# Performance work log

Measured on AMD Instinct MI355X. Metric: run time of the kernel, lower is better.

The kernel has to match this reference:

```python
import jax, jax.numpy as jnp
import numpy as np
from jax import lax

B, D, H, W = 16, 256, 64, 64
P = 8  # patchsize
EPS = 1e-5


def setup_inputs() -> dict:
    key = jax.random.key(0)
    ks = jax.random.split(key, 8)
    s = 0.02
    return {
        "x": jax.random.normal(ks[0], (B, D, H, W), jnp.float32),
        "wq": jax.random.normal(ks[1], (D, D), jnp.float32) * s,
        "bq": jnp.zeros((D,), jnp.float32),
        "wk": jax.random.normal(ks[2], (D, D), jnp.float32) * s,
        "bk": jnp.zeros((D,), jnp.float32),
        "wv": jax.random.normal(ks[3], (D, D), jnp.float32) * s,
        "bv": jnp.zeros((D,), jnp.float32),
        "w_out": jax.random.normal(ks[4], (D, D, 3, 3), jnp.float32) * s,
        "b_out": jnp.zeros((D,), jnp.float32),
        "gamma": jnp.ones((D,), jnp.float32),
        "beta": jnp.zeros((D,), jnp.float32),
        "bn_mean": jnp.zeros((D,), jnp.float32),
        "bn_var": jnp.ones((D,), jnp.float32),
    }


def _conv1x1(x, w, b):
    # x: [b,c,h,w], w: [o,c] (1x1 conv) -> [b,o,h,w]
    return jnp.einsum('bchw,oc->bohw', x, w) + b[None, :, None, None]


def _to_patches(t, p):
    # [b,d,h,w] -> [b, p*p, d*hh*ww]  (matches view+permute(0,2,4,1,3,5)+view)
    b, d, h, w = t.shape
    hh, ww = h // p, w // p
    t = t.reshape(b, d, p, hh, p, ww).transpose(0, 2, 4, 1, 3, 5)
    return t.reshape(b, p * p, d * hh * ww)


def reference(x, wq, bq, wk, bk, wv, bv, w_out, b_out, gamma, beta, bn_mean, bn_var):
    b, d, h, w = x.shape
    p = P
    hh, ww = h // p, w // p

    q = _to_patches(_conv1x1(x, wq, bq), p)  # [b, p^2, d*hh*ww]
    k = _to_patches(_conv1x1(x, wk, bk), p)
    v = _to_patches(_conv1x1(x, wv, bv), p)

    scale = 1.0 / jnp.sqrt(jnp.asarray(q.shape[-1], q.dtype))
    scores = jnp.einsum('bqe,bke->bqk', q, k) * scale  # [b, p^2, p^2]
    attn = jax.nn.softmax(scores, axis=-1)
    out = jnp.einsum('bqk,bke->bqe', attn, v)  # [b, p^2, d*hh*ww]

    # [b,p,p,d,hh,ww] -> permute(0,3,1,4,2,5) -> [b,d,h,w]
    out = out.reshape(b, p, p, d, hh, ww).transpose(0, 3, 1, 4, 2, 5).reshape(b, d, h, w)

    # 3x3 conv, padding 1
    y = lax.conv_general_dilated(out, w_out, window_strides=(1, 1),
                                 padding=((1, 1), (1, 1)),
                                 dimension_numbers=('NCHW', 'OIHW', 'NCHW'))
    y = y + b_out[None, :, None, None]

    # BatchNorm2d (eval mode with running stats)
    inv = gamma / jnp.sqrt(bn_var + EPS)
    y = (y - bn_mean[None, :, None, None]) * inv[None, :, None, None] + beta[None, :, None, None]

    # LeakyReLU(0.2)
    return jnp.where(y >= 0, y, 0.2 * y)
```

## Files before the change

### kernel.cpp

```cpp
#include <hip/hip_runtime.h>
#include <hip/hip_bf16.h>

#define BB 16
#define SS 4096

typedef __attribute__((ext_vector_type(8))) short short8;
typedef __attribute__((ext_vector_type(4))) float float4v;

__global__ __launch_bounds__(256) void wprep_qkv(
    const float* __restrict__ wq, const float* __restrict__ wk,
    const float* __restrict__ wv, __hip_bfloat16* __restrict__ blob) {
  int chunk = blockIdx.x * 256 + threadIdx.x;
  int lane = chunk & 63;
  int ob = (chunk >> 6) & 15;
  int cb = (chunk >> 10) & 7;
  int which = chunk >> 13;
  const float* W = (which == 0) ? wq : (which == 1) ? wk : wv;
  int o = ob * 16 + (lane & 15);
  int c0 = cb * 32 + (lane >> 4) * 8;
  const float* p = W + o * 256 + c0;
  union { uint4 u; __hip_bfloat16 h[8]; } t;
#pragma unroll
  for (int j = 0; j < 8; ++j) t.h[j] = __float2bfloat16(p[j]);
  *reinterpret_cast<uint4*>(blob + (size_t)chunk * 8) = t.u;
}

__global__ __launch_bounds__(256) void qkv_mfma(
    const float* __restrict__ x, const __hip_bfloat16* __restrict__ blob,
    const float* __restrict__ bq, const float* __restrict__ bk,
    const float* __restrict__ bv,
    __hip_bfloat16* __restrict__ qb, __hip_bfloat16* __restrict__ kb,
    __hip_bfloat16* __restrict__ vb) {
  __shared__ short ls[2][64 * 40];
  const int which = blockIdx.z;
  const int b = blockIdx.y;
  const int s0 = blockIdx.x * 64;
  const float* bias = (which == 0) ? bq : (which == 1) ? bk : bv;
  __hip_bfloat16* outb = (which == 0) ? qb : kb;
  const int tid = threadIdx.x;
  const int wave = tid >> 6, lane = tid & 63;
  const int q = lane >> 4, m = lane & 15;
  const int sl = tid & 63;
  const int cg = tid >> 6;
  float4v acc[4][4] = {};

  const float* xbase = x + ((size_t)(b * 256 + cg * 8)) * SS + s0 + sl;
  float xr[8];
#pragma unroll
  for (int i = 0; i < 8; ++i) xr[i] = xbase[(size_t)i * SS];
  {
    union { uint4 u; __hip_bfloat16 h[8]; } t;
#pragma unroll
    for (int i = 0; i < 8; ++i) t.h[i] = __float2bfloat16(xr[i]);
    *reinterpret_cast<uint4*>(&ls[0][sl * 40 + cg * 8]) = t.u;
  }
  __syncthreads();

  for (int cb = 0; cb < 8; ++cb) {
    const short* cur = ls[cb & 1];
    short* nxt = ls[(cb + 1) & 1];
    if (cb < 7) {
#pragma unroll
      for (int i = 0; i < 8; ++i)
        xr[i] = xbase[(size_t)(cb + 1) * 32 * SS + (size_t)i * SS];
    }
    short8 af[4];
#pragma unroll
    for (int of = 0; of < 4; ++of)
      af[of] = *reinterpret_cast<const short8*>(
          blob +
          ((size_t)(((which * 8 + cb) * 16 + wave * 4 + of) * 64 + lane)) * 8);
    short8 xf[4];
#pragma unroll
    for (int sf = 0; sf < 4; ++sf)
      xf[sf] =
          *reinterpret_cast<const short8*>(&cur[(sf * 16 + m) * 40 + q * 8]);
#pragma unroll
    for (int of = 0; of < 4; ++of)
#pragma unroll
      for (int sf = 0; sf < 4; ++sf)
        acc[of][sf] = __builtin_amdgcn_mfma_f32_16x16x32_bf16(
            af[of], xf[sf], acc[of][sf], 0, 0, 0);
    if (cb < 7) {
      union { uint4 u; __hip_bfloat16 h[8]; } t;
#pragma unroll
      for (int i = 0; i < 8; ++i) t.h[i] = __float2bfloat16(xr[i]);
      *reinterpret_cast<uint4*>(&nxt[sl * 40 + cg * 8]) = t.u;
    }
    __syncthreads();
  }
  if (which == 2) {
    const int h = s0 >> 6;
#pragma unroll
    for (int of = 0; of < 4; ++of) {
      int o_base = wave * 64 + of * 16 + q * 4;
#pragma unroll
      for (int sf = 0; sf < 4; ++sf) {
        int w = sf * 16 + m;
        union { uint2 u; __hip_bfloat16 hh[4]; } t;
#pragma unroll
        for (int r = 0; r < 4; ++r)
          t.hh[r] = __float2bfloat16(acc[of][sf][r] + bias[o_base + r]);
        *reinterpret_cast<uint2*>(
            vb + ((size_t)((b * 64 + h) * 64 + w)) * 256 + o_base) = t.u;
      }
    }
  } else {
#pragma unroll
    for (int of = 0; of < 4; ++of) {
      int o_base = wave * 64 + of * 16 + q * 4;
#pragma unroll
      for (int r = 0; r < 4; ++r) {
        int o = o_base + r;
        float bi = bias[o];
        __hip_bfloat16* op = outb + ((size_t)(b * 256 + o)) * SS + s0 + m;
#pragma unroll
        for (int sf = 0; sf < 4; ++sf)
          op[sf * 16] = __float2bfloat16(acc[of][sf][r] + bi);
      }
    }
  }
}

__global__ __launch_bounds__(256) void scores_mfma(
    const __hip_bfloat16* __restrict__ qb, const __hip_bfloat16* __restrict__ kb,
    float* __restrict__ part) {
  const int b = blockIdx.y;
  const int d0 = blockIdx.x * 8;
  const int tid = threadIdx.x;
  const int wave = tid >> 6, lane = tid & 63;
  const int q = lane >> 4, m = lane & 15;
  const int t = wave * 16 + m;
  const int arow = (t >> 3) * 8;
  const int acol = (t & 7) * 8;
  float4v acc[4] = {};

  for (int dd = 0; dd < 8; ++dd) {
    const int d = d0 + dd;
    const __hip_bfloat16* qp = qb + ((size_t)(b * 256 + d)) * SS;
    const __hip_bfloat16* kp = kb + ((size_t)(b * 256 + d)) * SS;
#pragma unroll
    for (int khalf = 0; khalf < 2; ++khalf) {
      const int oh = khalf * 4 + q;
      short8 af = *reinterpret_cast<const short8*>(
          qp + (arow + oh) * 64 + acol);
      short8 bf[4];
#pragma unroll
      for (int nt = 0; nt < 4; ++nt) {
        int tp = nt * 16 + m;
        bf[nt] = *reinterpret_cast<const short8*>(
            kp + ((tp >> 3) * 8 + oh) * 64 + (tp & 7) * 8);
      }
#pragma unroll
      for (int nt = 0; nt < 4; ++nt)
        acc[nt] = __builtin_amdgcn_mfma_f32_16x16x32_bf16(af, bf[nt], acc[nt],
                                                          0, 0, 0);
    }
  }
  float* pp = part + ((size_t)(blockIdx.x * BB + b)) * 4096;
#pragma unroll
  for (int nt = 0; nt < 4; ++nt)
#pragma unroll
    for (int r = 0; r < 4; ++r)
      pp[(wave * 16 + q * 4 + r) * 64 + nt * 16 + m] = acc[nt][r];
}

__global__ __launch_bounds__(64) void softmax_kernel(
    const float* __restrict__ part, __hip_bfloat16* __restrict__ attnb) {
  const int t = blockIdx.x;
  const int b = blockIdx.y;
  const int lane = threadIdx.x;
  float v = 0.f;
#pragma unroll
  for (int sl = 0; sl < 32; ++sl)
    v += part[((size_t)(sl * BB + b)) * 4096 + t * 64 + lane];
  v *= 0.0078125f;
  float m = v;
#pragma unroll
  for (int off = 32; off >= 1; off >>= 1) m = fmaxf(m, __shfl_xor(m, off));
  float e = __expf(v - m);
  float s = e;
#pragma unroll
  for (int off = 32; off >= 1; off >>= 1) s += __shfl_xor(s, off);
  attnb[(b * 64 + t) * 64 + lane] = __float2bfloat16(e / s);
}

__global__ __launch_bounds__(256) void apply_mfma(
    const __hip_bfloat16* __restrict__ attnb, const __hip_bfloat16* __restrict__ vb,
    __hip_bfloat16* __restrict__ zb) {
  __shared__ short Vs[64][268];
  const int off = blockIdx.x;
  const int b = blockIdx.y;
  const int oh = off >> 3, ow = off & 7;
  const int tid = threadIdx.x;
#pragma unroll
  for (int i = 0; i < 8; ++i) {
    int chunk = i * 256 + tid;
    int tp = chunk >> 5;
    int cg = chunk & 31;
    int hh = (tp >> 3) * 8 + oh;
    int wwp = (tp & 7) * 8 + ow;
    uint4 val = *reinterpret_cast<const uint4*>(
        vb + ((size_t)((b * 64 + hh) * 64 + wwp)) * 256 + cg * 8);
    *reinterpret_cast<uint4*>(&Vs[tp][cg * 8]) = val;
  }
  __syncthreads();
  const int wave = tid >> 6, lane = tid & 63;
  const int q = lane >> 4, m = lane & 15;
  float4v acc[4][4] = {};
#pragma unroll
  for (int ks = 0; ks < 2; ++ks) {
    short8 af[4];
#pragma unroll
    for (int mt = 0; mt < 4; ++mt)
      af[mt] = *reinterpret_cast<const short8*>(
          attnb + (b * 64 + mt * 16 + m) * 64 + ks * 32 + q * 8);
    short8 bf[4];
#pragma unroll
    for (int nt = 0; nt < 4; ++nt) {
      int d = wave * 64 + nt * 16 + m;
      union { short8 v; short s[8]; } t;
#pragma unroll
      for (int j = 0; j < 8; ++j) t.s[j] = Vs[ks * 32 + q * 8 + j][d];
      bf[nt] = t.v;
    }
#pragma unroll
    for (int mt = 0; mt < 4; ++mt)
#pragma unroll
      for (int nt = 0; nt < 4; ++nt)
        acc[mt][nt] = __builtin_amdgcn_mfma_f32_16x16x32_bf16(
            af[mt], bf[nt], acc[mt][nt], 0, 0, 0);
  }
#pragma unroll
  for (int mt = 0; mt < 4; ++mt)
#pragma unroll
    for (int r = 0; r < 4; ++r) {
      int t = mt * 16 + q * 4 + r;
      int h = (t >> 3) * 8 + oh;
      int w = (t & 7) * 8 + ow;
      __hip_bfloat16* base = zb + ((size_t)((b * 64 + h) * 64 + w)) * 256;
#pragma unroll
      for (int nt = 0; nt < 4; ++nt)
        base[wave * 64 + nt * 16 + m] = __float2bfloat16(acc[mt][nt][r]);
    }
}

__global__ __launch_bounds__(256) void wprep(
    const float* __restrict__ wo, __hip_bfloat16* __restrict__ blob) {
  int chunk = blockIdx.x * 256 + threadIdx.x;
  int l = chunk & 63;
  int ob = (chunk >> 6) & 15;
  int cb = (chunk >> 10) & 7;
  int tap = chunk >> 13;
  int o = ob * 16 + (l & 15);
  int c0 = cb * 32 + (l >> 4) * 8;
  union { uint4 u; __hip_bfloat16 h[8]; } t;
#pragma unroll
  for (int j = 0; j < 8; ++j)
    t.h[j] = __float2bfloat16(wo[((size_t)(o * 256 + c0 + j)) * 9 + tap]);
  *reinterpret_cast<uint4*>(blob + (size_t)chunk * 8) = t.u;
}

__global__ __launch_bounds__(256) void conv_mfma(
    const __hip_bfloat16* __restrict__ z, const __hip_bfloat16* __restrict__ blob,
    const float* __restrict__ bo, const float* __restrict__ gm,
    const float* __restrict__ bt, const float* __restrict__ mn,
    const float* __restrict__ vr, float* __restrict__ out) {
  __shared__ short zs[2][3 * 66 * 40];
  const int idx0 = blockIdx.x;
  const int h = (idx0 & 7) * 8 + ((idx0 >> 3) & 7);
  const int b = idx0 >> 6;
  const int tid = threadIdx.x;
  const int wave = tid >> 6, lane = tid & 63;
  const int q = lane >> 4, m = lane & 15;
  float4v acc[4][4] = {};

  int s_r[4], s_wp[4], s_cg[4];
  bool s_ok[4], s_act[4];
  const __hip_bfloat16* s_base[4];
#pragma unroll
  for (int k = 0; k < 4; ++k) {
    int idx = tid + k * 256;
    bool act = idx < 792;
    int cg = idx & 3;
    int t2 = idx >> 2;
    int wpos = act ? (t2 % 66) : 0;
    int r = act ? (t2 / 66) : 0;
    int h_in = h - 1 + r;
    int w_in = wpos - 1;
    bool ok = act && h_in >= 0 && h_in < 64 && w_in >= 0 && w_in < 64;
    if (!act) { r = 0; wpos = 0; cg = 0; }
    s_r[k] = r; s_wp[k] = wpos; s_cg[k] = cg;
    s_ok[k] = ok; s_act[k] = act;
    s_base[k] = z + ((size_t)((b * 64 + h_in) * 64 + w_in)) * 256 + cg * 8;
  }

  uint4 pf[4];
#pragma unroll
  for (int k = 0; k < 4; ++k)
    pf[k] = s_ok[k] ? *reinterpret_cast<const uint4*>(s_base[k])
                    : make_uint4(0u, 0u, 0u, 0u);
#pragma unroll
  for (int k = 0; k < 4; ++k)
    if (s_act[k])
      *reinterpret_cast<uint4*>(
          &zs[0][(s_r[k] * 66 + s_wp[k]) * 40 + s_cg[k] * 8]) = pf[k];

  short8 wfb[2][4];
#pragma unroll
  for (int of = 0; of < 4; ++of)
    wfb[0][of] = *reinterpret_cast<const short8*>(
        blob + ((size_t)((0 * 16 + wave * 4 + of) * 64 + lane)) * 8);
  __syncthreads();

#pragma unroll 2
  for (int cb = 0; cb < 8; ++cb) {
    const short* cur = zs[cb & 1];
    short* nxt = zs[(cb + 1) & 1];
    if (cb < 7) {
#pragma unroll
      for (int k = 0; k < 4; ++k)
        pf[k] = s_ok[k] ? *reinterpret_cast<const uint4*>(
                              s_base[k] + (size_t)(cb + 1) * 32)
                        : make_uint4(0u, 0u, 0u, 0u);
    }
#pragma unroll
    for (int tap = 0; tap < 9; ++tap) {
      const int kh = tap / 3, kw = tap % 3;
      const int p = (cb + tap) & 1;
      {
        const int ntap = (tap == 8) ? 0 : tap + 1;
        const int ncb = (tap == 8) ? cb + 1 : cb;
        if (ncb < 8) {
#pragma unroll
          for (int of = 0; of < 4; ++of)
            wfb[p ^ 1][of] = *reinterpret_cast<const short8*>(
                blob +
                ((size_t)(((ntap * 8 + ncb) * 16 + wave * 4 + of) * 64 + lane)) *
                    8);
        }
      }
      short8 zf[4];
#pragma unroll
      for (int wfi = 0; wfi < 4; ++wfi) {
        int wpos = wfi * 16 + m + kw;
        zf[wfi] = *reinterpret_cast<const short8*>(
            &cur[(kh * 66 + wpos) * 40 + q * 8]);
      }
#pragma unroll
      for (int of = 0; of < 4; ++of)
#pragma unroll
        for (int wfi = 0; wfi < 4; ++wfi)
          acc[of][wfi] = __builtin_amdgcn_mfma_f32_16x16x32_bf16(
              wfb[p][of], zf[wfi], acc[of][wfi], 0, 0, 0);
    }
    if (cb < 7) {
#pragma unroll
      for (int k = 0; k < 4; ++k)
        if (s_act[k])
          *reinterpret_cast<uint4*>(
              &nxt[(s_r[k] * 66 + s_wp[k]) * 40 + s_cg[k] * 8]) = pf[k];
    }
    __syncthreads();
  }
#pragma unroll
  for (int of = 0; of < 4; ++of) {
    int o_base = wave * 64 + of * 16 + q * 4;
#pragma unroll
    for (int r = 0; r < 4; ++r) {
      int o = o_base + r;
      float sc = gm[o] * rsqrtf(vr[o] + 1e-5f);
      float sh = bt[o] + (bo[o] - mn[o]) * sc;
#pragma unroll
      for (int wfi = 0; wfi < 4; ++wfi) {
        float y = acc[of][wfi][r] * sc + sh;
        y = (y >= 0.f) ? y : 0.2f * y;
        out[(((size_t)(b * 256 + o)) * 64 + h) * 64 + wfi * 16 + m] = y;
      }
    }
  }
}

extern "C" void kernel_launch(void* const* d_in, const int* in_sizes, int n_in,
                              void* d_out, int out_size, void* d_ws,
                              size_t ws_size, hipStream_t stream) {
  (void)in_sizes; (void)n_in; (void)out_size; (void)ws_size;
  const float* x  = (const float*)d_in[0];
  const float* wq = (const float*)d_in[1];
  const float* bq = (const float*)d_in[2];
  const float* wk = (const float*)d_in[3];
  const float* bk = (const float*)d_in[4];
  const float* wv = (const float*)d_in[5];
  const float* bv = (const float*)d_in[6];
  const float* wo = (const float*)d_in[7];
  const float* bo = (const float*)d_in[8];
  const float* gm = (const float*)d_in[9];
  const float* bt = (const float*)d_in[10];
  const float* mn = (const float*)d_in[11];
  const float* vr = (const float*)d_in[12];
  float* out = (float*)d_out;

  char* ws = (char*)d_ws;
  __hip_bfloat16* qb = (__hip_bfloat16*)(ws);
  __hip_bfloat16* kb = (__hip_bfloat16*)(ws + 33554432);
  __hip_bfloat16* attnb = (__hip_bfloat16*)(ws + 67371008);
  __hip_bfloat16* blob = (__hip_bfloat16*)(ws + 67502080);
  __hip_bfloat16* vb = (__hip_bfloat16*)d_out;
  __hip_bfloat16* blob_a = (__hip_bfloat16*)((char*)d_out + 33554432);
  float* part = (float*)((char*)d_out + 37748736);

  wprep<<<288, 256, 0, stream>>>(wo, blob);
  wprep_qkv<<<96, 256, 0, stream>>>(wq, wk, wv, blob_a);
  qkv_mfma<<<dim3(64, BB, 3), 256, 0, stream>>>(x, blob_a, bq, bk, bv,
                                                qb, kb, vb);
  scores_mfma<<<dim3(32, BB), 256, 0, stream>>>(qb, kb, part);
  softmax_kernel<<<dim3(64, BB), 64, 0, stream>>>(part, attnb);
  apply_mfma<<<dim3(64, BB), 256, 0, stream>>>(attnb, vb, qb );
  conv_mfma<<<dim3(BB * 64), 256, 0, stream>>>(qb, blob, bo, gm, bt, mn, vr,
                                               out);
}
```

Measured before the change: 314.6 us.

## Merge weight-prep kernels, fold softmax into scores via last-block counter, vectorize Q/K stores

Merges the two weight-conversion kernels into one launch that also zeroes per-batch counters. The softmax kernel is removed: each scores block bumps an atomic counter for its batch, and the last of the 32 blocks reduces the partial scores and writes the softmax itself. In qkv_mfma the MFMA operands are swapped for the Q/K path so each lane holds four consecutive spatial positions and can write 8-byte packed bf16 stores instead of scattered 2-byte ones. This saves two launches and improves store coalescing, but the softmax now runs serially in only one block per batch and reads partials through atomics.

```diff
diff --git a/kernel.cpp b/kernel.cpp
--- a/kernel.cpp
+++ b/kernel.cpp
@@ -7,22 +7,42 @@
 typedef __attribute__((ext_vector_type(8))) short short8;
 typedef __attribute__((ext_vector_type(4))) float float4v;
 
-__global__ __launch_bounds__(256) void wprep_qkv(
-    const float* __restrict__ wq, const float* __restrict__ wk,
-    const float* __restrict__ wv, __hip_bfloat16* __restrict__ blob) {
-  int chunk = blockIdx.x * 256 + threadIdx.x;
-  int lane = chunk & 63;
-  int ob = (chunk >> 6) & 15;
-  int cb = (chunk >> 10) & 7;
-  int which = chunk >> 13;
-  const float* W = (which == 0) ? wq : (which == 1) ? wk : wv;
-  int o = ob * 16 + (lane & 15);
-  int c0 = cb * 32 + (lane >> 4) * 8;
-  const float* p = W + o * 256 + c0;
-  union { uint4 u; __hip_bfloat16 h[8]; } t;
-#pragma unroll
-  for (int j = 0; j < 8; ++j) t.h[j] = __float2bfloat16(p[j]);
-  *reinterpret_cast<uint4*>(blob + (size_t)chunk * 8) = t.u;
+__global__ __launch_bounds__(256) void wprep_all(
+    const float* __restrict__ wo, const float* __restrict__ wq,
+    const float* __restrict__ wk, const float* __restrict__ wv,
+    __hip_bfloat16* __restrict__ blob, __hip_bfloat16* __restrict__ blob_a,
+    int* __restrict__ counters) {
+  const int bid = blockIdx.x;
+  const int tid = threadIdx.x;
+  if (bid == 383 && tid < BB) counters[tid] = 0;
+  if (bid < 288) {
+    int chunk = bid * 256 + tid;
+    int l = chunk & 63;
+    int ob = (chunk >> 6) & 15;
+    int cb = (chunk >> 10) & 7;
+    int tap = chunk >> 13;
+    int o = ob * 16 + (l & 15);
+    int c0 = cb * 32 + (l >> 4) * 8;
+    union { uint4 u; __hip_bfloat16 h[8]; } t;
+#pragma unroll
+    for (int j = 0; j < 8; ++j)
+      t.h[j] = __float2bfloat16(wo[((size_t)(o * 256 + c0 + j)) * 9 + tap]);
+    *reinterpret_cast<uint4*>(blob + (size_t)chunk * 8) = t.u;
+  } else {
+    int chunk = (bid - 288) * 256 + tid;
+    int lane = chunk & 63;
+    int ob = (chunk >> 6) & 15;
+    int cb = (chunk >> 10) & 7;
+    int which = chunk >> 13;
+    const float* W = (which == 0) ? wq : (which == 1) ? wk : wv;
+    int o = ob * 16 + (lane & 15);
+    int c0 = cb * 32 + (lane >> 4) * 8;
+    const float* p = W + o * 256 + c0;
+    union { uint4 u; __hip_bfloat16 h[8]; } t;
+#pragma unroll
+    for (int j = 0; j < 8; ++j) t.h[j] = __float2bfloat16(p[j]);
+    *reinterpret_cast<uint4*>(blob_a + (size_t)chunk * 8) = t.u;
+  }
 }
 
 __global__ __launch_bounds__(256) void qkv_mfma(
@@ -75,12 +95,21 @@
     for (int sf = 0; sf < 4; ++sf)
       xf[sf] =
           *reinterpret_cast<const short8*>(&cur[(sf * 16 + m) * 40 + q * 8]);
-#pragma unroll
-    for (int of = 0; of < 4; ++of)
-#pragma unroll
-      for (int sf = 0; sf < 4; ++sf)
-        acc[of][sf] = __builtin_amdgcn_mfma_f32_16x16x32_bf16(
-            af[of], xf[sf], acc[of][sf], 0, 0, 0);
+    if (which == 2) {
+#pragma unroll
+      for (int of = 0; of < 4; ++of)
+#pragma unroll
+        for (int sf = 0; sf < 4; ++sf)
+          acc[of][sf] = __builtin_amdgcn_mfma_f32_16x16x32_bf16(
+              af[of], xf[sf], acc[of][sf], 0, 0, 0);
+    } else {
+#pragma unroll
+      for (int of = 0; of < 4; ++of)
+#pragma unroll
+        for (int sf = 0; sf < 4; ++sf)
+          acc[of][sf] = __builtin_amdgcn_mfma_f32_16x16x32_bf16(
+              xf[sf], af[of], acc[of][sf], 0, 0, 0);
+    }
     if (cb < 7) {
       union { uint4 u; __hip_bfloat16 h[8]; } t;
 #pragma unroll
@@ -108,15 +137,16 @@
   } else {
 #pragma unroll
     for (int of = 0; of < 4; ++of) {
-      int o_base = wave * 64 + of * 16 + q * 4;
-#pragma unroll
-      for (int r = 0; r < 4; ++r) {
-        int o = o_base + r;
-        float bi = bias[o];
-        __hip_bfloat16* op = outb + ((size_t)(b * 256 + o)) * SS + s0 + m;
-#pragma unroll
-        for (int sf = 0; sf < 4; ++sf)
-          op[sf * 16] = __float2bfloat16(acc[of][sf][r] + bi);
+      int o = wave * 64 + of * 16 + m;
+      float bi = bias[o];
+      __hip_bfloat16* op = outb + (size_t)(b * 256 + o) * SS + s0;
+#pragma unroll
+      for (int sf = 0; sf < 4; ++sf) {
+        union { uint2 u; __hip_bfloat16 hh[4]; } t;
+#pragma unroll
+        for (int r = 0; r < 4; ++r)
+          t.hh[r] = __float2bfloat16(acc[of][sf][r] + bi);
+        *reinterpret_cast<uint2*>(op + sf * 16 + q * 4) = t.u;
       }
     }
   }
@@ -124,7 +154,8 @@
 
 __global__ __launch_bounds__(256) void scores_mfma(
     const __hip_bfloat16* __restrict__ qb, const __hip_bfloat16* __restrict__ kb,
-    float* __restrict__ part) {
+    float* __restrict__ part, __hip_bfloat16* __restrict__ attnb,
+    int* __restrict__ counters) {
   const int b = blockIdx.y;
   const int d0 = blockIdx.x * 8;
   const int tid = threadIdx.x;
@@ -163,26 +194,34 @@
 #pragma unroll
     for (int r = 0; r < 4; ++r)
       pp[(wave * 16 + q * 4 + r) * 64 + nt * 16 + m] = acc[nt][r];
-}
-
-__global__ __launch_bounds__(64) void softmax_kernel(
-    const float* __restrict__ part, __hip_bfloat16* __restrict__ attnb) {
-  const int t = blockIdx.x;
-  const int b = blockIdx.y;
-  const int lane = threadIdx.x;
-  float v = 0.f;
-#pragma unroll
-  for (int sl = 0; sl < 32; ++sl)
-    v += part[((size_t)(sl * BB + b)) * 4096 + t * 64 + lane];
-  v *= 0.0078125f;
-  float m = v;
-#pragma unroll
-  for (int off = 32; off >= 1; off >>= 1) m = fmaxf(m, __shfl_xor(m, off));
-  float e = __expf(v - m);
-  float s = e;
-#pragma unroll
-  for (int off = 32; off >= 1; off >>= 1) s += __shfl_xor(s, off);
-  attnb[(b * 64 + t) * 64 + lane] = __float2bfloat16(e / s);
+
+  __shared__ int lastf;
+  __syncthreads();
+  if (tid == 0) {
+    __threadfence();
+    int old = atomicAdd(&counters[b], 1);
+    lastf = (old == 31);
+  }
+  __syncthreads();
+  if (!lastf) return;
+
+  for (int i = 0; i < 16; ++i) {
+    int tt = wave * 16 + i;
+    float v = 0.f;
+#pragma unroll
+    for (int sl = 0; sl < 32; ++sl)
+      v += atomicAdd(&part[((size_t)(sl * BB + b)) * 4096 + tt * 64 + lane],
+                     0.f);
+    v *= 0.0078125f;
+    float mx = v;
+#pragma unroll
+    for (int off = 32; off >= 1; off >>= 1) mx = fmaxf(mx, __shfl_xor(mx, off));
+    float e = __expf(v - mx);
+    float s = e;
+#pragma unroll
+    for (int off = 32; off >= 1; off >>= 1) s += __shfl_xor(s, off);
+    attnb[(b * 64 + tt) * 64 + lane] = __float2bfloat16(e / s);
+  }
 }
 
 __global__ __launch_bounds__(256) void apply_mfma(
@@ -243,22 +282,6 @@
       for (int nt = 0; nt < 4; ++nt)
         base[wave * 64 + nt * 16 + m] = __float2bfloat16(acc[mt][nt][r]);
     }
-}
-
-__global__ __launch_bounds__(256) void wprep(
-    const float* __restrict__ wo, __hip_bfloat16* __restrict__ blob) {
-  int chunk = blockIdx.x * 256 + threadIdx.x;
-  int l = chunk & 63;
-  int ob = (chunk >> 6) & 15;
-  int cb = (chunk >> 10) & 7;
-  int tap = chunk >> 13;
-  int o = ob * 16 + (l & 15);
-  int c0 = cb * 32 + (l >> 4) * 8;
-  union { uint4 u; __hip_bfloat16 h[8]; } t;
-#pragma unroll
-  for (int j = 0; j < 8; ++j)
-    t.h[j] = __float2bfloat16(wo[((size_t)(o * 256 + c0 + j)) * 9 + tap]);
-  *reinterpret_cast<uint4*>(blob + (size_t)chunk * 8) = t.u;
 }
 
 __global__ __launch_bounds__(256) void conv_mfma(
@@ -403,18 +426,17 @@
   char* ws = (char*)d_ws;
   __hip_bfloat16* qb = (__hip_bfloat16*)(ws);
   __hip_bfloat16* kb = (__hip_bfloat16*)(ws + 33554432);
+  int* counters = (int*)(ws + 67108864);
   __hip_bfloat16* attnb = (__hip_bfloat16*)(ws + 67371008);
   __hip_bfloat16* blob = (__hip_bfloat16*)(ws + 67502080);
   __hip_bfloat16* vb = (__hip_bfloat16*)d_out;
   __hip_bfloat16* blob_a = (__hip_bfloat16*)((char*)d_out + 33554432);
   float* part = (float*)((char*)d_out + 37748736);
 
-  wprep<<<288, 256, 0, stream>>>(wo, blob);
-  wprep_qkv<<<96, 256, 0, stream>>>(wq, wk, wv, blob_a);
+  wprep_all<<<384, 256, 0, stream>>>(wo, wq, wk, wv, blob, blob_a, counters);
   qkv_mfma<<<dim3(64, BB, 3), 256, 0, stream>>>(x, blob_a, bq, bk, bv,
                                                 qb, kb, vb);
-  scores_mfma<<<dim3(32, BB), 256, 0, stream>>>(qb, kb, part);
-  softmax_kernel<<<dim3(64, BB), 64, 0, stream>>>(part, attnb);
+  scores_mfma<<<dim3(32, BB), 256, 0, stream>>>(qb, kb, part, attnb, counters);
   apply_mfma<<<dim3(64, BB), 256, 0, stream>>>(attnb, vb, qb );
   conv_mfma<<<dim3(BB * 64), 256, 0, stream>>>(qb, blob, bo, gm, bt, mn, vr,
                                                out);
```

Measured after the change: 401.5 us. +27.6%, slower.
